# Kernel optimization log

Hardware: AMD Instinct MI355X
Metric: run time of the kernel (lower is better)

Reference implementation:

```python
import jax, jax.numpy as jnp
import numpy as np

N = 4096          # n_nodes
M = 8192          # m_nodes (= 2*N, required by block structure)
D = 128           # in_dim == hidden_dim (conv1 is reapplied to its own output)
H = 128
NUM_ITERS = 3


def setup_inputs() -> dict:
    key = jax.random.key(0)
    ks = jax.random.split(key, 6)
    X = jax.random.normal(ks[0], (N, D), dtype=jnp.float32)
    R = jax.random.uniform(ks[1], (N, N), dtype=jnp.float32)
    A = 0.5 * (R + R.T)  # symmetric, strictly positive connectivity matrix
    # upsample MLP: Linear(n_nodes -> m_nodes - n_nodes), torch weight layout [out, in]
    W_up = jax.random.normal(ks[2], (M - N, N), dtype=jnp.float32) * 0.02
    b_up = jnp.zeros((M - N,), dtype=jnp.float32)
    # GCNConv linear weights stored [in, out]
    W1 = jax.random.normal(ks[3], (D, H), dtype=jnp.float32) * 0.05
    b1 = jnp.zeros((H,), dtype=jnp.float32)
    W2 = jax.random.normal(ks[4], (H, H), dtype=jnp.float32) * 0.05
    b2 = jnp.zeros((H,), dtype=jnp.float32)
    return dict(X=X, A=A, W_up=W_up, b_up=b_up, W1=W1, b1=b1, W2=W2, b2=b2)


def _gcn(Adj, X, W, b):
    # PyG GCNConv on a fully dense, strictly-positive weighted graph:
    # every diagonal entry is nonzero, so add_remaining_self_loops is a no-op and
    # out = D^{-1/2} A D^{-1/2} (X W) + b  exactly.
    deg = Adj.sum(axis=0)                         # [m] column degree
    dinv = jnp.where(deg > 0, jax.lax.rsqrt(deg), 0.0)
    An = Adj * dinv[:, None] * dinv[None, :]      # symmetric normalization
    return An @ (X @ W) + b


def reference(X, A, W_up, b_up, W1, b1, W2, b2):
    # new_nodes = upsample_mlp(X.T).T  -> [M-N, D]
    new_nodes = (X.T @ W_up.T + b_up).T
    Xu = jnp.concatenate([X, new_nodes], axis=0)  # [M, D]
    # block adjacency: [[A, A.T], [A, sigmoid(new @ new.T)]]
    Adj = jnp.block([[A, A.T],
                     [A, jax.nn.sigmoid(new_nodes @ new_nodes.T)]])  # [M, M]
    A_out = Adj
    for _ in range(NUM_ITERS):
        Xu = jax.nn.relu(_gcn(Adj, Xu, W1, b1))
        Adj = jax.nn.sigmoid(Xu @ Xu.T)           # mid-loop adjacency rebuild
        Xu = jax.nn.relu(_gcn(Adj, Xu, W2, b2))
        A_out = jax.nn.sigmoid(Xu @ Xu.T)
        # NOTE: edge_index for the next conv1 is NOT rebuilt from A_out in the
        # original (only after conv1), so Adj carries the mid-loop matrix.
    return A_out
```

## Files before the change

kernel.cpp:

```cpp
#include <hip/hip_runtime.h>
#include <hip/hip_bf16.h>


#define N_NODES 4096
#define M_NODES 8192
#define DIM 128
#define SLICE_ELEMS ((size_t)M_NODES * DIM)

typedef __attribute__((ext_vector_type(4))) float f32x4;
typedef __attribute__((ext_vector_type(8))) short bf16x8;

__device__ __forceinline__ unsigned short f2bf(float f) {
  union { float f; unsigned u; } v; v.f = f;
  unsigned r = v.u + 0x7fffu + ((v.u >> 16) & 1u);
  return (unsigned short)(r >> 16);
}

__device__ __forceinline__ void gld16(unsigned short* lds, const unsigned short* g) {
  __builtin_amdgcn_global_load_lds(
      (const __attribute__((address_space(1))) unsigned int*)g,
      (__attribute__((address_space(3))) unsigned int*)lds, 16, 0, 0);
}

__device__ __forceinline__ float sigmoidf_(float x) { return 1.0f / (1.0f + __expf(-x)); }


__global__ void cast_x_kernel(const float* __restrict__ X, unsigned short* __restrict__ Xu,
                              unsigned short* __restrict__ XT,
                              float* __restrict__ colsumA) {
  int idx = blockIdx.x * 256 + threadIdx.x;
  if (idx < N_NODES) colsumA[idx] = 0.f;
  int i = idx >> 7, c = idx & 127;
  unsigned short b = f2bf(X[idx]);
  Xu[idx] = b;
  XT[(size_t)c * N_NODES + i] = b;
}

__global__ void cast_wt2_kernel(const float* __restrict__ W1, const float* __restrict__ W2,
                                unsigned short* __restrict__ WT1,
                                unsigned short* __restrict__ WT2) {
  int idx = blockIdx.x * 256 + threadIdx.x;
  const float* W = idx < 16384 ? W1 : W2;
  unsigned short* WT = idx < 16384 ? WT1 : WT2;
  int j = idx & 16383;
  int k = j >> 7, c = j & 127;
  WT[c * DIM + k] = f2bf(W[j]);
}

__global__ void cast_a_kernel(const float* __restrict__ A, unsigned short* __restrict__ Adj,
                              float* __restrict__ colsumA) {
  int c = blockIdx.x * 256 + threadIdx.x;
  int r0 = blockIdx.y * 128;
  int tm = r0 >> 7;
  int kc = c >> 10, st = (c & 1023) >> 5, e = c & 31;
  size_t a1 = ((size_t)(tm)      * 8 + kc)     * 131072 + (size_t)st * 4096 + e;
  size_t a2 = ((size_t)(tm)      * 8 + 4 + kc) * 131072 + (size_t)st * 4096 + e;
  size_t a3 = ((size_t)(tm + 32) * 8 + kc)     * 131072 + (size_t)st * 4096 + e;
  float s = 0.f;
  for (int r = 0; r < 128; ++r) {
    float a = A[(size_t)(r0 + r) * N_NODES + c];
    unsigned short b = f2bf(a);
    Adj[a1 + r * 32] = b; Adj[a2 + r * 32] = b; Adj[a3 + r * 32] = b;
    s += a;
  }
  atomicAdd(&colsumA[c], s);
}

__global__ void init_deg_kernel(const float* __restrict__ colsumA, float* __restrict__ deg) {
  int i = blockIdx.x * 256 + threadIdx.x;
  deg[i] = (i < N_NODES) ? 2.0f * colsumA[i] : colsumA[i - N_NODES];
}


__global__ __launch_bounds__(256, 2)
void agg64_kernel(const unsigned short* __restrict__ At,
                  const unsigned short* __restrict__ BT, long ldb,
                  float* __restrict__ accBase, int kIters) {
  __shared__ __align__(16) unsigned short smem[18432];
  const int t = threadIdx.x, w = t >> 6, lane = t & 63;
  const int q = lane >> 4, l15 = lane & 15;
  const int sx = (l15 >> 1) & 3;
  const int wm = w & 1, wn = w >> 1;
  const int tm = blockIdx.x >> 1;
  const int h2048 = (blockIdx.x & 1) * 2048;
  const int sg0 = blockIdx.y * kIters;
  const int arow = t >> 2;
  const int xchk = (t & 3) ^ ((t >> 3) & 3);

  auto STAGE = [&](int s, int b) {
    unsigned short* la = smem + b * 6144;
    unsigned short* lb = la + 2048;
    int sg = sg0 + s;
    size_t aaddr = ((size_t)tm * 8 + (sg >> 5)) * 131072 + (size_t)(sg & 31) * 4096 + h2048;
    gld16(&la[t * 8],        &At[aaddr + arow * 32 + xchk * 8]);
    gld16(&lb[t * 8],        &BT[(size_t)arow * ldb + (size_t)sg * 32 + xchk * 8]);
    gld16(&lb[2048 + t * 8], &BT[(size_t)(64 + arow) * ldb + (size_t)sg * 32 + xchk * 8]);
  };

  f32x4 acc[2][4];
#pragma unroll
  for (int a = 0; a < 2; ++a)
#pragma unroll
    for (int b = 0; b < 4; ++b) acc[a][b] = (f32x4)0.f;

  STAGE(0, 0);
  STAGE(1, 1);

  for (int s = 0; s < kIters; ++s) {
    if (s + 2 < kIters) {
      STAGE(s + 2, (s + 2) % 3);
      asm volatile("s_waitcnt vmcnt(6)" ::: "memory");
    } else if (s + 1 < kIters) {
      asm volatile("s_waitcnt vmcnt(3)" ::: "memory");
    } else {
      asm volatile("s_waitcnt vmcnt(0)" ::: "memory");
    }
    __builtin_amdgcn_s_barrier();
    __builtin_amdgcn_sched_barrier(0);

    const unsigned short* la = smem + (s % 3) * 6144;
    const unsigned short* lb = la + 2048;
    bf16x8 a0 = *(const bf16x8*)&la[(wm * 32 + l15) * 32 + (q ^ sx) * 8];
    bf16x8 a1 = *(const bf16x8*)&la[(wm * 32 + 16 + l15) * 32 + (q ^ sx) * 8];
#pragma unroll
    for (int nt = 0; nt < 4; ++nt) {
      bf16x8 b = *(const bf16x8*)&lb[(wn * 64 + nt * 16 + l15) * 32 + (q ^ sx) * 8];
      acc[0][nt] = __builtin_amdgcn_mfma_f32_16x16x32_bf16(a0, b, acc[0][nt], 0, 0, 0);
      acc[1][nt] = __builtin_amdgcn_mfma_f32_16x16x32_bf16(a1, b, acc[1][nt], 0, 0, 0);
    }
    __builtin_amdgcn_sched_barrier(0);
    __builtin_amdgcn_s_barrier();
    __builtin_amdgcn_sched_barrier(0);
  }
  float* ct = accBase + (size_t)blockIdx.y * SLICE_ELEMS + (size_t)blockIdx.x * 8192;
#pragma unroll
  for (int mt = 0; mt < 2; ++mt)
#pragma unroll
    for (int nt = 0; nt < 4; ++nt)
      *(f32x4*)&ct[((w * 8 + mt * 4 + nt) * 256) + (q * 16 + l15) * 4] = acc[mt][nt];
}


__global__ __launch_bounds__(256)
void up_agg_f32(const float* __restrict__ Wup, const unsigned short* __restrict__ BT,
                float* __restrict__ accBase) {
  __shared__ __align__(16) unsigned short smem[6144];
  unsigned short* la = smem;
  unsigned short* lb = smem + 2048;
  const int t = threadIdx.x, w = t >> 6, lane = t & 63;
  const int q = lane >> 4, l15 = lane & 15;
  const int r0 = blockIdx.x * 64;
  const int k0 = blockIdx.y * 512;
  const int arow = t >> 2, achk = t & 3;

  f32x4 acc[8];
#pragma unroll
  for (int b = 0; b < 8; ++b) acc[b] = (f32x4)0.f;

  for (int s = 0; s < 16; ++s) {
    int kb = k0 + s * 32;
    __syncthreads();
    gld16(&lb[t * 8],        &BT[(size_t)arow * N_NODES + kb + achk * 8]);
    gld16(&lb[2048 + t * 8], &BT[(size_t)(64 + arow) * N_NODES + kb + achk * 8]);
    const float* ap = &Wup[(size_t)(r0 + (t >> 2)) * N_NODES + kb + (t & 3) * 8];
    float4 v0 = *(const float4*)ap;
    float4 v1 = *(const float4*)(ap + 4);
    ushort4 o0, o1;
    o0.x = f2bf(v0.x); o0.y = f2bf(v0.y); o0.z = f2bf(v0.z); o0.w = f2bf(v0.w);
    o1.x = f2bf(v1.x); o1.y = f2bf(v1.y); o1.z = f2bf(v1.z); o1.w = f2bf(v1.w);
    *(ushort4*)&la[t * 8] = o0;
    *(ushort4*)&la[t * 8 + 4] = o1;
    __syncthreads();

    bf16x8 a0 = *(const bf16x8*)&la[(w * 16 + l15) * 32 + q * 8];
#pragma unroll
    for (int nt = 0; nt < 8; ++nt) {
      bf16x8 b = *(const bf16x8*)&lb[(nt * 16 + l15) * 32 + q * 8];
      acc[nt] = __builtin_amdgcn_mfma_f32_16x16x32_bf16(a0, b, acc[nt], 0, 0, 0);
    }
  }
  float* ct = accBase + (size_t)blockIdx.y * SLICE_ELEMS + (size_t)blockIdx.x * 8192;
#pragma unroll
  for (int nt = 0; nt < 8; ++nt)
    *(f32x4*)&ct[((w * 8 + nt) * 256) + (q * 16 + l15) * 4] = acc[nt];
}

__global__ void reduce64_kernel(const float* __restrict__ acc,
                                unsigned short* __restrict__ dst,
                                const float* __restrict__ bias_row,
                                const float* __restrict__ bias_col,
                                const float* __restrict__ deg, int mode, int nSlices) {
  int p = blockIdx.x * 256 + threadIdx.x;
  float s = 0.f;
  for (int sp = 0; sp < nSlices; ++sp) s += acc[(size_t)sp * SLICE_ELEMS + p];
  int tile = p >> 13, r = p & 8191;
  int grp = r >> 8;
  int r2 = r & 255;
  int i = r2 & 3, ql = r2 >> 2;
  int row, col;
  float v;
  if (mode == 0) {
    int w = grp >> 3, nt = grp & 7;
    row = tile * 64 + w * 16 + (ql >> 4) * 4 + i;
    col = nt * 16 + (ql & 15);
    v = s + bias_row[row];
  } else {
    int w = grp >> 3, mt = (grp >> 2) & 1, nt = grp & 3;
    row = tile * 64 + (w & 1) * 32 + mt * 16 + (ql >> 4) * 4 + i;
    col = (w >> 1) * 64 + nt * 16 + (ql & 15);
    float d = deg[row];
    float dv = d > 0.f ? rsqrtf(d) : 0.f;
    v = fmaxf(dv * s + bias_col[col], 0.f);
  }
  dst[(size_t)row * DIM + col] = f2bf(v);
}


template <int MODE>
__global__ __launch_bounds__(256)
void rebuild_kernel(const unsigned short* __restrict__ XA,
                    const unsigned short* __restrict__ XB,
                    void* __restrict__ out, long p1 ,
                    long col0, float* __restrict__ deg, int nB) {
  __shared__ __align__(16) unsigned short smem[34816];
  __shared__ float lcol[128];
  __shared__ float lrow[128];
  unsigned short* lA = smem;
  unsigned short* lB = smem + 16384;
  const int t = threadIdx.x, w = t >> 6, lane = t & 63;
  const int q = lane >> 4, l15 = lane & 15;
  const int sx = (l15 >> 1) & 3;

  int rem = blockIdx.x, bi = 0;
  while (rem >= nB - bi) { rem -= nB - bi; ++bi; }
  const int bj = bi + rem;
  const int i0 = bi * 128, j0 = bj * 128;
  const bool offdiag = (bi != bj);

  const int srow = t >> 2;
  const int xchk = (t & 3) ^ ((t >> 3) & 3);
#pragma unroll
  for (int kk = 0; kk < 4; ++kk)
#pragma unroll
    for (int h = 0; h < 2; ++h) {
      gld16(&lA[kk * 4096 + h * 2048 + t * 8],
            &XA[(size_t)(i0 + h * 64 + srow) * DIM + kk * 32 + xchk * 8]);
      gld16(&lB[kk * 4096 + h * 2048 + t * 8],
            &XB[(size_t)(j0 + h * 64 + srow) * DIM + kk * 32 + xchk * 8]);
    }
  if (MODE == 0 && t < 128) { lcol[t] = 0.f; lrow[t] = 0.f; }
  __syncthreads();

  f32x4 acc[2][8];
#pragma unroll
  for (int a = 0; a < 2; ++a)
#pragma unroll
    for (int b = 0; b < 8; ++b) acc[a][b] = (f32x4)0.f;

#pragma unroll
  for (int kk = 0; kk < 4; ++kk) {
    bf16x8 a0 = *(const bf16x8*)&lA[kk * 4096 + (w * 32 + l15) * 32 + ((q ^ sx)) * 8];
    bf16x8 a1 = *(const bf16x8*)&lA[kk * 4096 + (w * 32 + 16 + l15) * 32 + ((q ^ sx)) * 8];
#pragma unroll
    for (int nt = 0; nt < 8; ++nt) {
      bf16x8 b = *(const bf16x8*)&lB[kk * 4096 + (nt * 16 + l15) * 32 + ((q ^ sx)) * 8];
      acc[0][nt] = __builtin_amdgcn_mfma_f32_16x16x32_bf16(a0, b, acc[0][nt], 0, 0, 0);
      acc[1][nt] = __builtin_amdgcn_mfma_f32_16x16x32_bf16(a1, b, acc[1][nt], 0, 0, 0);
    }
  }
  __syncthreads();

  if (MODE == 0) {
    unsigned short* lC  = smem;
    unsigned short* lCt = smem + 17408;
    float rs[2][4] = {{0.f, 0.f, 0.f, 0.f}, {0.f, 0.f, 0.f, 0.f}};
#pragma unroll
    for (int mt = 0; mt < 2; ++mt)
#pragma unroll
      for (int nt = 0; nt < 8; ++nt) {
        float cs = 0.f;
#pragma unroll
        for (int i = 0; i < 4; ++i) {
          float sv = sigmoidf_(acc[mt][nt][i]);
          cs += sv;
          unsigned short hb = f2bf(sv);
          int row = w * 32 + mt * 16 + q * 4 + i, colL = nt * 16 + l15;
          lC[row * 136 + colL] = hb;
          if (offdiag) { lCt[colL * 136 + row] = hb; rs[mt][i] += sv; }
        }
        cs += __shfl_xor(cs, 16);
        cs += __shfl_xor(cs, 32);
        if (lane < 16) atomicAdd(&lcol[nt * 16 + lane], cs);
      }
    if (offdiag) {
#pragma unroll
      for (int mt = 0; mt < 2; ++mt)
#pragma unroll
        for (int i = 0; i < 4; ++i) {
          float v = rs[mt][i];
          v += __shfl_xor(v, 1); v += __shfl_xor(v, 2);
          v += __shfl_xor(v, 4); v += __shfl_xor(v, 8);
          if (l15 == 0) atomicAdd(&lrow[w * 32 + mt * 16 + q * 4 + i], v);
        }
    }
    __syncthreads();
    unsigned short* og = (unsigned short*)out;
    {
      const long rowbase = p1 + i0, colbase = col0 + j0;
      const size_t tb = ((size_t)(rowbase >> 7) * 8 + (colbase >> 10)) * 131072;
      const int stb = (int)((colbase & 1023) >> 5);
#pragma unroll
      for (int cc = 0; cc < 8; ++cc) {
        int ch = t + cc * 256;
        int row = ch >> 4, c16 = ch & 15;
        *(bf16x8*)&og[tb + (size_t)(stb + (c16 >> 2)) * 4096 + row * 32 + (c16 & 3) * 8] =
            *(const bf16x8*)&lC[row * 136 + c16 * 8];
      }
    }
    if (offdiag) {
      const long rowbase = p1 + j0, colbase = col0 + i0;
      const size_t tb = ((size_t)(rowbase >> 7) * 8 + (colbase >> 10)) * 131072;
      const int stb = (int)((colbase & 1023) >> 5);
#pragma unroll
      for (int cc = 0; cc < 8; ++cc) {
        int ch = t + cc * 256;
        int row = ch >> 4, c16 = ch & 15;
        *(bf16x8*)&og[tb + (size_t)(stb + (c16 >> 2)) * 4096 + row * 32 + (c16 & 3) * 8] =
            *(const bf16x8*)&lCt[row * 136 + c16 * 8];
      }
    }
    if (t < 128) atomicAdd(&deg[col0 + j0 + t], lcol[t]);
    if (offdiag && t < 128) atomicAdd(&deg[col0 + i0 + t], lrow[t]);
  } else {
    float* og = (float*)out;
    float* lCf = (float*)smem;
#pragma unroll
    for (int mt = 0; mt < 2; ++mt)
#pragma unroll
      for (int nt = 0; nt < 8; ++nt)
#pragma unroll
        for (int i = 0; i < 4; ++i) acc[mt][nt][i] = sigmoidf_(acc[mt][nt][i]);
#pragma unroll
    for (int h2 = 0; h2 < 2; ++h2) {
      __syncthreads();
      if ((w >> 1) == h2) {
#pragma unroll
        for (int mt = 0; mt < 2; ++mt)
#pragma unroll
          for (int nt = 0; nt < 8; ++nt)
#pragma unroll
            for (int i = 0; i < 4; ++i)
              lCf[((w & 1) * 32 + mt * 16 + q * 4 + i) * 132 + nt * 16 + l15] =
                  acc[mt][nt][i];
      }
      __syncthreads();
#pragma unroll
      for (int j = 0; j < 8; ++j) {
        int ch = t + j * 256;
        int r64 = ch >> 5, c4 = (ch & 31) * 4;
        *(f32x4*)&og[(size_t)(i0 + h2 * 64 + r64) * p1 + j0 + c4] =
            *(const f32x4*)&lCf[r64 * 132 + c4];
      }
    }
    if (offdiag) {
#pragma unroll
      for (int h2 = 0; h2 < 2; ++h2) {
        __syncthreads();
#pragma unroll
        for (int mt = 0; mt < 2; ++mt)
#pragma unroll
          for (int nt = 0; nt < 8; ++nt)
            if ((nt >> 2) == h2) {
#pragma unroll
              for (int i = 0; i < 4; ++i)
                lCf[((nt & 3) * 16 + l15) * 132 + (w * 32 + mt * 16 + q * 4 + i)] =
                    acc[mt][nt][i];
            }
        __syncthreads();
#pragma unroll
        for (int j = 0; j < 8; ++j) {
          int ch = t + j * 256;
          int r64 = ch >> 5, c4 = (ch & 31) * 4;
          *(f32x4*)&og[(size_t)(j0 + h2 * 64 + r64) * p1 + i0 + c4] =
              *(const f32x4*)&lCf[r64 * 132 + c4];
        }
      }
    }
  }
}


__global__ __launch_bounds__(256)
void yz_kernel(const unsigned short* __restrict__ Xu, const unsigned short* __restrict__ WT,
               const float* __restrict__ deg, unsigned short* __restrict__ ZT, int ldz,
               float* __restrict__ zbuf) {
  __shared__ __align__(16) unsigned short smem[32768];
  unsigned short* lA = smem;
  unsigned short* lB = smem + 16384;
  const int t = threadIdx.x, w = t >> 6, lane = t & 63;
  const int q = lane >> 4, l15 = lane & 15;
  const int sx = (l15 >> 1) & 3;
  const int r0 = blockIdx.x * 128;
  if (zbuf) {
    int gid = blockIdx.x * 256 + t;
    if (gid < M_NODES) zbuf[gid] = 0.f;
  }
  const int srow = t >> 2;
  const int xchk = (t & 3) ^ ((t >> 3) & 3);
#pragma unroll
  for (int kk = 0; kk < 4; ++kk)
#pragma unroll
    for (int h = 0; h < 2; ++h) {
      gld16(&lA[kk * 4096 + h * 2048 + t * 8],
            &Xu[(size_t)(r0 + h * 64 + srow) * DIM + kk * 32 + xchk * 8]);
      gld16(&lB[kk * 4096 + h * 2048 + t * 8],
            &WT[(size_t)(h * 64 + srow) * DIM + kk * 32 + xchk * 8]);
    }
  __syncthreads();

  f32x4 acc[2][8];
#pragma unroll
  for (int a = 0; a < 2; ++a)
#pragma unroll
    for (int b = 0; b < 8; ++b) acc[a][b] = (f32x4)0.f;

#pragma unroll
  for (int kk = 0; kk < 4; ++kk) {
    bf16x8 a0 = *(const bf16x8*)&lA[kk * 4096 + (w * 32 + l15) * 32 + (q ^ sx) * 8];
    bf16x8 a1 = *(const bf16x8*)&lA[kk * 4096 + (w * 32 + 16 + l15) * 32 + (q ^ sx) * 8];
#pragma unroll
    for (int nt = 0; nt < 8; ++nt) {
      bf16x8 b = *(const bf16x8*)&lB[kk * 4096 + (nt * 16 + l15) * 32 + (q ^ sx) * 8];
      acc[0][nt] = __builtin_amdgcn_mfma_f32_16x16x32_bf16(a0, b, acc[0][nt], 0, 0, 0);
      acc[1][nt] = __builtin_amdgcn_mfma_f32_16x16x32_bf16(a1, b, acc[1][nt], 0, 0, 0);
    }
  }
  __syncthreads();
  unsigned short* lT = smem;
#pragma unroll
  for (int mt = 0; mt < 2; ++mt)
#pragma unroll
    for (int i = 0; i < 4; ++i) {
      int r = w * 32 + mt * 16 + q * 4 + i;
      float d = deg[r0 + r];
      float dv = d > 0.f ? rsqrtf(d) : 0.f;
#pragma unroll
      for (int nt = 0; nt < 8; ++nt)
        lT[(nt * 16 + l15) * 136 + r] = f2bf(dv * acc[mt][nt][i]);
    }
  __syncthreads();
#pragma unroll
  for (int cc = 0; cc < 8; ++cc) {
    int ch = t + cc * 256;
    int c = ch >> 4, c16 = ch & 15;
    *(bf16x8*)&ZT[(size_t)c * ldz + r0 + c16 * 8] = *(const bf16x8*)&lT[c * 136 + c16 * 8];
  }
}


extern "C" void kernel_launch(void* const* d_in, const int* in_sizes, int n_in,
                              void* d_out, int out_size, void* d_ws, size_t ws_size,
                              hipStream_t stream) {
  (void)in_sizes; (void)n_in; (void)out_size;
  const float* X   = (const float*)d_in[0];
  const float* A   = (const float*)d_in[1];
  const float* Wup = (const float*)d_in[2];
  const float* bup = (const float*)d_in[3];
  const float* W1  = (const float*)d_in[4];
  const float* b1  = (const float*)d_in[5];
  const float* W2  = (const float*)d_in[6];
  const float* b2  = (const float*)d_in[7];

  const size_t ADJ_BYTES = (size_t)M_NODES * M_NODES * 2;
  char* ws = (char*)d_ws;
  size_t off = 0;
  auto alloc = [&](size_t bytes) {
    char* p = ws + off;
    off += (bytes + 255) & ~(size_t)255;
    return p;
  };
  float*          accb    = (float*)alloc(8 * SLICE_ELEMS * 4);
  unsigned short* Xu      = (unsigned short*)alloc((size_t)M_NODES * DIM * 2);
  unsigned short* ZT      = (unsigned short*)alloc((size_t)DIM * M_NODES * 2);
  unsigned short* XT      = (unsigned short*)alloc((size_t)DIM * N_NODES * 2);
  unsigned short* W1T     = (unsigned short*)alloc(DIM * DIM * 2);
  unsigned short* W2T     = (unsigned short*)alloc(DIM * DIM * 2);
  float*          colsumA = (float*)alloc(N_NODES * 4);
  float*          degA    = (float*)alloc(M_NODES * 4);
  float*          degB    = (float*)alloc(M_NODES * 4);

  unsigned short* Adj;
  if (ws_size >= off + ADJ_BYTES) Adj = (unsigned short*)(ws + off);
  else                            Adj = (unsigned short*)d_out;

  unsigned short* XuNew = Xu + (size_t)N_NODES * DIM;

  cast_x_kernel<<<N_NODES * DIM / 256, 256, 0, stream>>>(X, Xu, XT, colsumA);
  cast_wt2_kernel<<<128, 256, 0, stream>>>(W1, W2, W1T, W2T);

  up_agg_f32<<<dim3(N_NODES / 64, 8), 256, 0, stream>>>(Wup, XT, accb);
  reduce64_kernel<<<N_NODES * DIM / 256, 256, 0, stream>>>(
      accb, XuNew, bup, nullptr, nullptr, 0, 8);

  cast_a_kernel<<<dim3(N_NODES / 256, N_NODES / 128), 256, 0, stream>>>(A, Adj, colsumA);
  init_deg_kernel<<<M_NODES / 256, 256, 0, stream>>>(colsumA, degA);
  rebuild_kernel<0><<<32 * 33 / 2, 256, 0, stream>>>(
      XuNew, XuNew, Adj, N_NODES, N_NODES, degA, 32);

  float* degCur = degA;
  float* degMid = degB;
  for (int it = 0; it < 3; ++it) {
    yz_kernel<<<M_NODES / 128, 256, 0, stream>>>(Xu, W1T, degCur, ZT, M_NODES, degMid);
    agg64_kernel<<<dim3(M_NODES / 64, 4), 256, 0, stream>>>(Adj, ZT, M_NODES, accb, 64);
    reduce64_kernel<<<M_NODES * DIM / 256, 256, 0, stream>>>(
        accb, Xu, nullptr, b1, degCur, 1, 4);
    rebuild_kernel<0><<<64 * 65 / 2, 256, 0, stream>>>(
        Xu, Xu, Adj, 0, 0, degMid, 64);
    yz_kernel<<<M_NODES / 128, 256, 0, stream>>>(Xu, W2T, degMid, ZT, M_NODES, nullptr);
    agg64_kernel<<<dim3(M_NODES / 64, 4), 256, 0, stream>>>(Adj, ZT, M_NODES, accb, 64);
    reduce64_kernel<<<M_NODES * DIM / 256, 256, 0, stream>>>(
        accb, Xu, nullptr, b2, degMid, 1, 4);
    if (it == 2)
      rebuild_kernel<1><<<64 * 65 / 2, 256, 0, stream>>>(
          Xu, Xu, d_out, M_NODES, 0, nullptr, 64);
    float* tmp = degCur; degCur = degMid; degMid = tmp;
  }
}
```

Baseline: 901.7 us.

## Enlarge aggregation GEMM tile to 128 rows with K=64 stages and split-K 8

Replaces the 64x128 aggregation kernel with a 128x128 tile that loads 64-wide K chunks per stage using an XOR swizzle, double-buffered instead of triple-buffered. Each A/B stage is reused across more MFMAs, cutting loads of ZT per output row. Split-K rises from 4 to 8 slices, so the reduce kernel sums more partial buffers and is re-indexed for the new accumulator layout. LDS use per block grows to 64KB, which may limit occupancy.

```diff
diff --git a/kernel.cpp b/kernel.cpp
--- a/kernel.cpp
+++ b/kernel.cpp
@@ -73,71 +73,74 @@
 
 
 __global__ __launch_bounds__(256, 2)
-void agg64_kernel(const unsigned short* __restrict__ At,
-                  const unsigned short* __restrict__ BT, long ldb,
-                  float* __restrict__ accBase, int kIters) {
-  __shared__ __align__(16) unsigned short smem[18432];
+void agg128_kernel(const unsigned short* __restrict__ At,
+                   const unsigned short* __restrict__ BT, long ldb,
+                   float* __restrict__ accBase, int kIters) {
+  __shared__ __align__(16) unsigned short smem[32768];
   const int t = threadIdx.x, w = t >> 6, lane = t & 63;
   const int q = lane >> 4, l15 = lane & 15;
-  const int sx = (l15 >> 1) & 3;
-  const int wm = w & 1, wn = w >> 1;
-  const int tm = blockIdx.x >> 1;
-  const int h2048 = (blockIdx.x & 1) * 2048;
-  const int sg0 = blockIdx.y * kIters;
-  const int arow = t >> 2;
-  const int xchk = (t & 3) ^ ((t >> 3) & 3);
+  const int xk = l15 & 7;
+  const int tm = blockIdx.x;
+  const int sg0 = blockIdx.y * (kIters * 2);
+  const size_t kbase = (size_t)sg0 * 32;
 
   auto STAGE = [&](int s, int b) {
-    unsigned short* la = smem + b * 6144;
-    unsigned short* lb = la + 2048;
-    int sg = sg0 + s;
-    size_t aaddr = ((size_t)tm * 8 + (sg >> 5)) * 131072 + (size_t)(sg & 31) * 4096 + h2048;
-    gld16(&la[t * 8],        &At[aaddr + arow * 32 + xchk * 8]);
-    gld16(&lb[t * 8],        &BT[(size_t)arow * ldb + (size_t)sg * 32 + xchk * 8]);
-    gld16(&lb[2048 + t * 8], &BT[(size_t)(64 + arow) * ldb + (size_t)sg * 32 + xchk * 8]);
+    unsigned short* la = smem + b * 16384;
+    unsigned short* lb = la + 8192;
+#pragma unroll
+    for (int j = 0; j < 4; ++j) {
+      int ch = j * 256 + t;
+      int row = ch >> 3, phys = ch & 7;
+      int c = phys ^ (row & 7);
+      int sg = sg0 + 2 * s + (c >> 2);
+      gld16(&la[ch * 8],
+            &At[((size_t)tm * 8 + (sg >> 5)) * 131072 + (size_t)(sg & 31) * 4096 +
+                row * 32 + (c & 3) * 8]);
+      gld16(&lb[ch * 8], &BT[(size_t)row * ldb + kbase + s * 64 + c * 8]);
+    }
   };
 
-  f32x4 acc[2][4];
+  f32x4 acc[2][8];
 #pragma unroll
   for (int a = 0; a < 2; ++a)
 #pragma unroll
-    for (int b = 0; b < 4; ++b) acc[a][b] = (f32x4)0.f;
+    for (int b = 0; b < 8; ++b) acc[a][b] = (f32x4)0.f;
 
   STAGE(0, 0);
-  STAGE(1, 1);
 
   for (int s = 0; s < kIters; ++s) {
-    if (s + 2 < kIters) {
-      STAGE(s + 2, (s + 2) % 3);
-      asm volatile("s_waitcnt vmcnt(6)" ::: "memory");
-    } else if (s + 1 < kIters) {
-      asm volatile("s_waitcnt vmcnt(3)" ::: "memory");
+    if (s + 1 < kIters) {
+      STAGE(s + 1, (s + 1) & 1);
+      asm volatile("s_waitcnt vmcnt(8)" ::: "memory");
     } else {
       asm volatile("s_waitcnt vmcnt(0)" ::: "memory");
     }
     __builtin_amdgcn_s_barrier();
     __builtin_amdgcn_sched_barrier(0);
 
-    const unsigned short* la = smem + (s % 3) * 6144;
-    const unsigned short* lb = la + 2048;
-    bf16x8 a0 = *(const bf16x8*)&la[(wm * 32 + l15) * 32 + (q ^ sx) * 8];
-    bf16x8 a1 = *(const bf16x8*)&la[(wm * 32 + 16 + l15) * 32 + (q ^ sx) * 8];
-#pragma unroll
-    for (int nt = 0; nt < 4; ++nt) {
-      bf16x8 b = *(const bf16x8*)&lb[(wn * 64 + nt * 16 + l15) * 32 + (q ^ sx) * 8];
-      acc[0][nt] = __builtin_amdgcn_mfma_f32_16x16x32_bf16(a0, b, acc[0][nt], 0, 0, 0);
-      acc[1][nt] = __builtin_amdgcn_mfma_f32_16x16x32_bf16(a1, b, acc[1][nt], 0, 0, 0);
+    const unsigned short* la = smem + (s & 1) * 16384;
+    const unsigned short* lb = la + 8192;
+#pragma unroll
+    for (int kk = 0; kk < 2; ++kk) {
+      bf16x8 a0 = *(const bf16x8*)&la[(w * 32 + l15) * 64 + (((kk << 2) + q) ^ xk) * 8];
+      bf16x8 a1 = *(const bf16x8*)&la[(w * 32 + 16 + l15) * 64 + (((kk << 2) + q) ^ xk) * 8];
+#pragma unroll
+      for (int nt = 0; nt < 8; ++nt) {
+        bf16x8 b = *(const bf16x8*)&lb[(nt * 16 + l15) * 64 + (((kk << 2) + q) ^ xk) * 8];
+        acc[0][nt] = __builtin_amdgcn_mfma_f32_16x16x32_bf16(a0, b, acc[0][nt], 0, 0, 0);
+        acc[1][nt] = __builtin_amdgcn_mfma_f32_16x16x32_bf16(a1, b, acc[1][nt], 0, 0, 0);
+      }
     }
     __builtin_amdgcn_sched_barrier(0);
     __builtin_amdgcn_s_barrier();
     __builtin_amdgcn_sched_barrier(0);
   }
-  float* ct = accBase + (size_t)blockIdx.y * SLICE_ELEMS + (size_t)blockIdx.x * 8192;
+  float* ct = accBase + (size_t)blockIdx.y * SLICE_ELEMS + (size_t)blockIdx.x * 16384;
 #pragma unroll
   for (int mt = 0; mt < 2; ++mt)
 #pragma unroll
-    for (int nt = 0; nt < 4; ++nt)
-      *(f32x4*)&ct[((w * 8 + mt * 4 + nt) * 256) + (q * 16 + l15) * 4] = acc[mt][nt];
+    for (int nt = 0; nt < 8; ++nt)
+      *(f32x4*)&ct[((w * 16 + mt * 8 + nt) * 256) + (q * 16 + l15) * 4] = acc[mt][nt];
 }
 
 
@@ -193,21 +196,25 @@
   int p = blockIdx.x * 256 + threadIdx.x;
   float s = 0.f;
   for (int sp = 0; sp < nSlices; ++sp) s += acc[(size_t)sp * SLICE_ELEMS + p];
-  int tile = p >> 13, r = p & 8191;
-  int grp = r >> 8;
-  int r2 = r & 255;
-  int i = r2 & 3, ql = r2 >> 2;
   int row, col;
   float v;
   if (mode == 0) {
+    int tile = p >> 13, r = p & 8191;
+    int grp = r >> 8;
     int w = grp >> 3, nt = grp & 7;
+    int r2 = r & 255;
+    int i = r2 & 3, ql = r2 >> 2;
     row = tile * 64 + w * 16 + (ql >> 4) * 4 + i;
     col = nt * 16 + (ql & 15);
     v = s + bias_row[row];
   } else {
-    int w = grp >> 3, mt = (grp >> 2) & 1, nt = grp & 3;
-    row = tile * 64 + (w & 1) * 32 + mt * 16 + (ql >> 4) * 4 + i;
-    col = (w >> 1) * 64 + nt * 16 + (ql & 15);
+    int tile = p >> 14, r = p & 16383;
+    int grp = r >> 8;
+    int w = grp >> 4, mt = (grp >> 3) & 1, nt = grp & 7;
+    int r2 = r & 255;
+    int i = r2 & 3, ql = r2 >> 2;
+    row = tile * 128 + w * 32 + mt * 16 + (ql >> 4) * 4 + i;
+    col = nt * 16 + (ql & 15);
     float d = deg[row];
     float dv = d > 0.f ? rsqrtf(d) : 0.f;
     v = fmaxf(dv * s + bias_col[col], 0.f);
@@ -511,15 +518,15 @@
   float* degMid = degB;
   for (int it = 0; it < 3; ++it) {
     yz_kernel<<<M_NODES / 128, 256, 0, stream>>>(Xu, W1T, degCur, ZT, M_NODES, degMid);
-    agg64_kernel<<<dim3(M_NODES / 64, 4), 256, 0, stream>>>(Adj, ZT, M_NODES, accb, 64);
+    agg128_kernel<<<dim3(M_NODES / 128, 8), 256, 0, stream>>>(Adj, ZT, M_NODES, accb, 16);
     reduce64_kernel<<<M_NODES * DIM / 256, 256, 0, stream>>>(
-        accb, Xu, nullptr, b1, degCur, 1, 4);
+        accb, Xu, nullptr, b1, degCur, 1, 8);
     rebuild_kernel<0><<<64 * 65 / 2, 256, 0, stream>>>(
         Xu, Xu, Adj, 0, 0, degMid, 64);
     yz_kernel<<<M_NODES / 128, 256, 0, stream>>>(Xu, W2T, degMid, ZT, M_NODES, nullptr);
-    agg64_kernel<<<dim3(M_NODES / 64, 4), 256, 0, stream>>>(Adj, ZT, M_NODES, accb, 64);
+    agg128_kernel<<<dim3(M_NODES / 128, 8), 256, 0, stream>>>(Adj, ZT, M_NODES, accb, 16);
     reduce64_kernel<<<M_NODES * DIM / 256, 256, 0, stream>>>(
-        accb, Xu, nullptr, b2, degMid, 1, 4);
+        accb, Xu, nullptr, b2, degMid, 1, 8);
     if (it == 2)
       rebuild_kernel<1><<<64 * 65 / 2, 256, 0, stream>>>(
           Xu, Xu, d_out, M_NODES, 0, nullptr, 64);
```

After: 905.2 us. No clear change (+0.4%).
